# Optimization experiments

Measured on AMD Instinct MI355X. Metric: run time of the kernel, lower is better.

## Reference

```python
import jax, jax.numpy as jnp
import numpy as np

D_MODEL = 1024
NUM_HEADS = 16
D_K = D_MODEL // NUM_HEADS


def setup_inputs() -> dict:
    key = jax.random.key(0)
    ks = jax.random.split(key, 11)
    B, S, D = 2, 2048, D_MODEL
    scale = 1.0 / np.sqrt(D)
    inp = {
        'query': jax.random.normal(ks[0], (B, S, D), jnp.float32),
        'key':   jax.random.normal(ks[1], (B, S, D), jnp.float32),
        'value': jax.random.normal(ks[2], (B, S, D), jnp.float32),
        'Wq': jax.random.normal(ks[3], (D, D), jnp.float32) * scale,
        'bq': jnp.zeros((D,), jnp.float32),
        'Wk': jax.random.normal(ks[4], (D, D), jnp.float32) * scale,
        'bk': jnp.zeros((D,), jnp.float32),
        'Wv': jax.random.normal(ks[5], (D, D), jnp.float32) * scale,
        'bv': jnp.zeros((D,), jnp.float32),
        'Wo': jax.random.normal(ks[6], (D, D), jnp.float32) * scale,
        'bo': jnp.zeros((D,), jnp.float32),
    }
    return inp


def reference(query, key, value, Wq, bq, Wk, bk, Wv, bv, Wo, bo):
    B, S, D = query.shape
    H, dk = NUM_HEADS, D_K
    # QKV projections (torch Linear: x @ W.T + b)
    Q = (query @ Wq.T + bq).reshape(B, S, H, dk).transpose(0, 2, 1, 3)  # [B,H,S,dk]
    K = (key   @ Wk.T + bk).reshape(B, S, H, dk).transpose(0, 2, 1, 3)
    V = (value @ Wv.T + bv).reshape(B, S, H, dk).transpose(0, 2, 1, 3)
    # scaled dot-product attention; note: scaling uses d_k = per-head dim
    scores = jnp.einsum('bhqd,bhkd->bhqk', Q, K) / jnp.sqrt(jnp.float32(dk))
    attn = jax.nn.softmax(scores, axis=-1)  # [B,H,S,S]
    out = jnp.einsum('bhqk,bhkd->bhqd', attn, V)  # [B,H,S,dk]
    out = out.transpose(0, 2, 1, 3).reshape(B, S, D)
    return out @ Wo.T + bo
```

## Files before the change

kernel.cpp:

```cpp
#include <hip/hip_runtime.h>
#include <hip/hip_bf16.h>

#define S_LEN 2048
#define DM 1024
#define NH 16
#define DKH 64
#define BATCH 2

typedef __attribute__((ext_vector_type(4))) float f32x4;
typedef __attribute__((ext_vector_type(8))) short s16x8;
typedef __attribute__((ext_vector_type(4))) short s16x4;

__device__ __forceinline__ unsigned short f2bf(float f) {
    union { __hip_bfloat16 h; unsigned short u; } cv;
    cv.h = __float2bfloat16(f);
    return cv.u;
}

__device__ __forceinline__ void gl_lds16(const unsigned short* g, unsigned short* l) {
    __builtin_amdgcn_global_load_lds(
        (const __attribute__((address_space(1))) unsigned int*)g,
        (__attribute__((address_space(3))) unsigned int*)l,
        16, 0, 0);
}

__global__ __launch_bounds__(256) void cast_w(
    const float* __restrict__ w0, const float* __restrict__ w1,
    const float* __restrict__ w2, const float* __restrict__ w3,
    unsigned short* __restrict__ dst)
{
    const float* s = (blockIdx.y == 0) ? w0 : (blockIdx.y == 1) ? w1 : (blockIdx.y == 2) ? w2 : w3;
    unsigned short* d = dst + (size_t)blockIdx.y * (1024 * 1024);
    const int i = (blockIdx.x * 256 + threadIdx.x) * 8;
    float4 a = *(const float4*)(s + i), b = *(const float4*)(s + i + 4);
    s16x8 v;
    v[0] = f2bf(a.x); v[1] = f2bf(a.y); v[2] = f2bf(a.z); v[3] = f2bf(a.w);
    v[4] = f2bf(b.x); v[5] = f2bf(b.y); v[6] = f2bf(b.z); v[7] = f2bf(b.w);
    *(s16x8*)(d + i) = v;
}

__global__ __launch_bounds__(256) void qkv_gemm(
    const float* __restrict__ xq, const float* __restrict__ xk, const float* __restrict__ xv,
    const unsigned short* __restrict__ Wb,
    const float* __restrict__ bq, const float* __restrict__ bk, const float* __restrict__ bv,
    unsigned short* __restrict__ Qb, unsigned short* __restrict__ Kb,
    unsigned short* __restrict__ Vt)
{
    __shared__ __align__(16) unsigned short Al[128 * 32];
    __shared__ __align__(16) unsigned short Bl[128 * 32];

    const int tid = threadIdx.x, lane = tid & 63, w = tid >> 6;
    const int bn = blockIdx.x;
    const int seg = bn >> 3;
    const int nl0 = (bn & 7) * 128;
    const int m0 = blockIdx.y * 128;

    const float* A           = (seg == 0) ? xq : (seg == 1) ? xk : xv;
    const unsigned short* W  = Wb + (size_t)seg * 1024 * 1024;
    const float* bias        = (seg == 0) ? bq : (seg == 1) ? bk : bv;

    const int ar = tid >> 1, ac = (tid & 1) * 16;
    const int br = lane >> 2, bc = (lane & 3) * 8;
    const int wm = (w >> 1) * 64, wn = (w & 1) * 64;

    f32x4 acc[4][4] = {};

    for (int k0 = 0; k0 < DM; k0 += 32) {
        __syncthreads();
        #pragma unroll
        for (int j = 0; j < 2; j++) {
            const unsigned short* g = W + (size_t)(nl0 + w * 32 + j * 16 + br) * DM + k0 + bc;
            gl_lds16(g, &Bl[(w * 32 + j * 16) * 32]);
        }
        {
            const float* s = A + (size_t)(m0 + ar) * DM + k0 + ac;
            float4 x0 = *(const float4*)s,       x1 = *(const float4*)(s + 4);
            float4 x2 = *(const float4*)(s + 8), x3 = *(const float4*)(s + 12);
            s16x8 lo, hi;
            lo[0]=f2bf(x0.x); lo[1]=f2bf(x0.y); lo[2]=f2bf(x0.z); lo[3]=f2bf(x0.w);
            lo[4]=f2bf(x1.x); lo[5]=f2bf(x1.y); lo[6]=f2bf(x1.z); lo[7]=f2bf(x1.w);
            hi[0]=f2bf(x2.x); hi[1]=f2bf(x2.y); hi[2]=f2bf(x2.z); hi[3]=f2bf(x2.w);
            hi[4]=f2bf(x3.x); hi[5]=f2bf(x3.y); hi[6]=f2bf(x3.z); hi[7]=f2bf(x3.w);
            *(s16x8*)&Al[ar * 32 + ac] = lo;
            *(s16x8*)&Al[ar * 32 + ac + 8] = hi;
        }
        __syncthreads();

        const int kk = (lane >> 4) << 3;
        s16x8 af[4], bfr[4];
        #pragma unroll
        for (int i = 0; i < 4; i++) af[i]  = *(const s16x8*)&Al[(wm + i * 16 + (lane & 15)) * 32 + kk];
        #pragma unroll
        for (int i = 0; i < 4; i++) bfr[i] = *(const s16x8*)&Bl[(wn + i * 16 + (lane & 15)) * 32 + kk];
        #pragma unroll
        for (int i = 0; i < 4; i++)
            #pragma unroll
            for (int j = 0; j < 4; j++)
                acc[i][j] = __builtin_amdgcn_mfma_f32_16x16x32_bf16(af[i], bfr[j], acc[i][j], 0, 0, 0);
    }

    float bvv[4];
    #pragma unroll
    for (int ni = 0; ni < 4; ni++) bvv[ni] = bias[nl0 + wn + ni * 16 + (lane & 15)];

    if (seg < 2) {
        unsigned short* O = (seg == 0) ? Qb : Kb;
        #pragma unroll
        for (int mi = 0; mi < 4; mi++) {
            const int r0 = m0 + wm + mi * 16 + ((lane >> 4) << 2);
            #pragma unroll
            for (int ni = 0; ni < 4; ni++) {
                const int cg = nl0 + wn + ni * 16 + (lane & 15);
                #pragma unroll
                for (int r = 0; r < 4; r++)
                    O[(size_t)(r0 + r) * DM + cg] = f2bf(acc[mi][ni][r] + bvv[ni]);
            }
        }
    } else {
        #pragma unroll
        for (int mi = 0; mi < 4; mi++) {
            const int r0 = m0 + wm + mi * 16 + ((lane >> 4) << 2);
            const int bb = r0 >> 11, ss = r0 & (S_LEN - 1);
            #pragma unroll
            for (int ni = 0; ni < 4; ni++) {
                const int cg = nl0 + wn + ni * 16 + (lane & 15);
                const int hh = cg >> 6, dd = cg & 63;
                s16x4 vv;
                #pragma unroll
                for (int r = 0; r < 4; r++) vv[r] = (short)f2bf(acc[mi][ni][r] + bvv[ni]);
                *(s16x4*)(Vt + ((size_t)(bb * NH + hh) * DKH + dd) * S_LEN + ss) = vv;
            }
        }
    }
}

__global__ __launch_bounds__(512) void attn_k(
    const unsigned short* Qb, const unsigned short* __restrict__ Kb,
    const unsigned short* __restrict__ Vt, unsigned short* ctx)
{
    constexpr int KP = 72;
    __shared__ __align__(16) unsigned short Kl[2][64 * KP];
    __shared__ __align__(16) unsigned short Vl[2][64 * KP];
    __shared__ __align__(16) unsigned short Pl[8][16 * KP];

    const int tid = threadIdx.x, lane = tid & 63, w = tid >> 6;
    const int b = blockIdx.z, h = blockIdx.y, q0 = blockIdx.x * 128;
    const size_t qkb = (size_t)b * S_LEN * DM + h * DKH;
    const size_t vtb = (size_t)(b * NH + h) * DKH * S_LEN;

    s16x8 qf[2];
    {
        const int qr = q0 + w * 16 + (lane & 15);
        const unsigned short* qp = Qb + qkb + (size_t)qr * DM + ((lane >> 4) << 3);
        qf[0] = *(const s16x8*)qp;
        qf[1] = *(const s16x8*)(qp + 32);
    }

    f32x4 o[4] = {};
    float lp[4] = {0.f, 0.f, 0.f, 0.f};
    const int sr = tid >> 3, sc = (tid & 7) * 8;

    const float K1 = 0.18033688011112042f;
    const float K2 = 17.31234049066756f;

    s16x8 kreg = *(const s16x8*)(Kb + qkb + (size_t)sr * DM + sc);
    s16x8 vreg = *(const s16x8*)(Vt + vtb + (size_t)sr * S_LEN + sc);
    *(s16x8*)&Kl[0][sr * KP + sc] = kreg;
    *(s16x8*)&Vl[0][sr * KP + sc] = vreg;
    __syncthreads();
    int cur = 0;

    for (int t = 0; t < S_LEN / 64; ++t) {
        if (t < S_LEN / 64 - 1) {
            kreg = *(const s16x8*)(Kb + qkb + (size_t)((t + 1) * 64 + sr) * DM + sc);
            vreg = *(const s16x8*)(Vt + vtb + (size_t)sr * S_LEN + (t + 1) * 64 + sc);
        }
        const int kk = (lane >> 4) << 3;
        f32x4 sv[4] = {};
        #pragma unroll
        for (int c = 0; c < 2; c++) {
            #pragma unroll
            for (int f = 0; f < 4; f++) {
                s16x8 kf = *(const s16x8*)&Kl[cur][(f * 16 + (lane & 15)) * KP + c * 32 + kk];
                sv[f] = __builtin_amdgcn_mfma_f32_16x16x32_bf16(qf[c], kf, sv[f], 0, 0, 0);
            }
        }
        float p[4][4];
        #pragma unroll
        for (int f = 0; f < 4; f++)
            #pragma unroll
            for (int r = 0; r < 4; r++)
                p[f][r] = exp2f(fmaf(sv[f][r], K1, -K2));
        #pragma unroll
        for (int r = 0; r < 4; r++)
            lp[r] += (p[0][r] + p[1][r]) + (p[2][r] + p[3][r]);
        #pragma unroll
        for (int f = 0; f < 4; f++)
            #pragma unroll
            for (int r = 0; r < 4; r++)
                Pl[w][(((lane >> 4) << 2) + r) * KP + f * 16 + (lane & 15)] = f2bf(p[f][r]);
        #pragma unroll
        for (int c = 0; c < 2; c++) {
            s16x8 pa = *(const s16x8*)&Pl[w][(lane & 15) * KP + c * 32 + kk];
            #pragma unroll
            for (int j = 0; j < 4; j++) {
                s16x8 vf = *(const s16x8*)&Vl[cur][(j * 16 + (lane & 15)) * KP + c * 32 + kk];
                o[j] = __builtin_amdgcn_mfma_f32_16x16x32_bf16(pa, vf, o[j], 0, 0, 0);
            }
        }
        if (t < S_LEN / 64 - 1) {
            *(s16x8*)&Kl[cur ^ 1][sr * KP + sc] = kreg;
            *(s16x8*)&Vl[cur ^ 1][sr * KP + sc] = vreg;
        }
        __syncthreads();
        cur ^= 1;
    }

    float inv[4];
    #pragma unroll
    for (int r = 0; r < 4; r++) {
        float l = lp[r];
        l += __shfl_xor(l, 1); l += __shfl_xor(l, 2);
        l += __shfl_xor(l, 4); l += __shfl_xor(l, 8);
        inv[r] = 1.0f / l;
    }
    #pragma unroll
    for (int r = 0; r < 4; r++)
        #pragma unroll
        for (int j = 0; j < 4; j++)
            Pl[w][(((lane >> 4) << 2) + r) * KP + j * 16 + (lane & 15)] = f2bf(o[j][r] * inv[r]);
    {
        const int rr = lane >> 2, cc = (lane & 3) * 16;
        s16x8 a  = *(const s16x8*)&Pl[w][rr * KP + cc];
        s16x8 b2 = *(const s16x8*)&Pl[w][rr * KP + cc + 8];
        unsigned short* cp = ctx + (size_t)b * S_LEN * DM + (size_t)(q0 + w * 16 + rr) * DM + h * DKH + cc;
        *(s16x8*)cp = a; *(s16x8*)(cp + 8) = b2;
    }
}

__global__ __launch_bounds__(256) void out_gemm(
    const unsigned short* __restrict__ ctx, const unsigned short* __restrict__ Wo2,
    const float* __restrict__ bo, float* __restrict__ out)
{
    __shared__ __align__(16) unsigned short Al[128 * 32];
    __shared__ __align__(16) unsigned short Bl[128 * 32];

    const int tid = threadIdx.x, lane = tid & 63, w = tid >> 6;
    const int wm = (w >> 1) * 64, wn = (w & 1) * 64;
    const int m0 = blockIdx.y * 128, n0 = blockIdx.x * 128;
    const int br = lane >> 2, bc = (lane & 3) * 8;

    f32x4 acc[4][4] = {};

    for (int k0 = 0; k0 < DM; k0 += 32) {
        __syncthreads();
        #pragma unroll
        for (int j = 0; j < 2; j++) {
            gl_lds16(ctx + (size_t)(m0 + w * 32 + j * 16 + br) * DM + k0 + bc,
                     &Al[(w * 32 + j * 16) * 32]);
            gl_lds16(Wo2 + (size_t)(n0 + w * 32 + j * 16 + br) * DM + k0 + bc,
                     &Bl[(w * 32 + j * 16) * 32]);
        }
        __syncthreads();

        const int kk = (lane >> 4) << 3;
        s16x8 af[4], bfr[4];
        #pragma unroll
        for (int i = 0; i < 4; i++) af[i]  = *(const s16x8*)&Al[(wm + i * 16 + (lane & 15)) * 32 + kk];
        #pragma unroll
        for (int i = 0; i < 4; i++) bfr[i] = *(const s16x8*)&Bl[(wn + i * 16 + (lane & 15)) * 32 + kk];
        #pragma unroll
        for (int i = 0; i < 4; i++)
            #pragma unroll
            for (int j = 0; j < 4; j++)
                acc[i][j] = __builtin_amdgcn_mfma_f32_16x16x32_bf16(af[i], bfr[j], acc[i][j], 0, 0, 0);
    }

    float bvv[4];
    #pragma unroll
    for (int ni = 0; ni < 4; ni++) bvv[ni] = bo[n0 + wn + ni * 16 + (lane & 15)];
    #pragma unroll
    for (int mi = 0; mi < 4; mi++) {
        const int r0 = m0 + wm + mi * 16 + ((lane >> 4) << 2);
        #pragma unroll
        for (int ni = 0; ni < 4; ni++) {
            const int cg = n0 + wn + ni * 16 + (lane & 15);
            #pragma unroll
            for (int r = 0; r < 4; r++)
                out[(size_t)(r0 + r) * DM + cg] = acc[mi][ni][r] + bvv[ni];
        }
    }
}

extern "C" void kernel_launch(void* const* d_in, const int* in_sizes, int n_in,
                              void* d_out, int out_size, void* d_ws, size_t ws_size,
                              hipStream_t stream) {
    const float* q  = (const float*)d_in[0];
    const float* k  = (const float*)d_in[1];
    const float* v  = (const float*)d_in[2];
    const float* Wq = (const float*)d_in[3];
    const float* bq = (const float*)d_in[4];
    const float* Wk = (const float*)d_in[5];
    const float* bk = (const float*)d_in[6];
    const float* Wv = (const float*)d_in[7];
    const float* bv = (const float*)d_in[8];
    const float* Wo = (const float*)d_in[9];
    const float* bo = (const float*)d_in[10];

    const size_t NE = (size_t)BATCH * S_LEN * DM;
    unsigned short* Kb = (unsigned short*)d_ws;
    unsigned short* Vt = Kb + NE;
    unsigned short* Qb = Vt + NE;
    unsigned short* Wb = Qb + NE;
    float* out = (float*)d_out;

    cast_w<<<dim3(512, 4), 256, 0, stream>>>(Wq, Wk, Wv, Wo, Wb);
    qkv_gemm<<<dim3(24, 32), 256, 0, stream>>>(q, k, v, Wb, bq, bk, bv, Qb, Kb, Vt);
    attn_k<<<dim3(16, NH, BATCH), 512, 0, stream>>>(Qb, Kb, Vt, Qb );
    out_gemm<<<dim3(8, 32), 256, 0, stream>>>(Qb , Wb + 3 * 1024 * 1024, bo, out);
}
```

Before: 263.4 us.

## Swizzle LDS layouts, async-load attention tiles, precast inputs, shrink output GEMM tile

Replaces the padded and unswizzled LDS layouts with XOR-swizzled layouts in every GEMM and in attention, which targets LDS bank conflicts. Attention now streams K/V tiles with direct global-to-LDS loads instead of going through registers, and raises wave priority around the MFMA sections. When the workspace is large enough, a separate kernel casts the inputs to bf16 so the QKV GEMM can use global_load_lds for both operands. The output GEMM tile is cut to 128x64 to launch more blocks. The extra cast pass adds a kernel launch and extra memory traffic, and the precast path only runs if the workspace size check passes.

Measured after the change: 243.7 us. 1.08x faster.

```diff
diff --git a/kernel.cpp b/kernel.cpp
--- a/kernel.cpp
+++ b/kernel.cpp
@@ -22,6 +22,22 @@
         (const __attribute__((address_space(1))) unsigned int*)g,
         (__attribute__((address_space(3))) unsigned int*)l,
         16, 0, 0);
+}
+
+__device__ __forceinline__ int a32(int row, int col) {
+    return row * 32 + ((((col >> 3) ^ ((row >> 1) & 3)) & 3) << 3) + (col & 7);
+}
+__device__ __forceinline__ int csw32(int l) {
+    return (((l & 3) ^ ((l >> 3) & 3)) << 3);
+}
+__device__ __forceinline__ int a64(int row, int col) {
+    return row * 64 + ((((col >> 3) ^ (row & 7)) & 7) << 3) + (col & 7);
+}
+__device__ __forceinline__ int csw64(int l) {
+    return (((l & 7) ^ ((l >> 3) & 7)) << 3);
+}
+__device__ __forceinline__ int pswz(int row, int col) {
+    return row * 72 + (col ^ ((row & 8) << 1));
 }
 
 __global__ __launch_bounds__(256) void cast_w(
@@ -39,7 +55,108 @@
     *(s16x8*)(d + i) = v;
 }
 
-__global__ __launch_bounds__(256) void qkv_gemm(
+__global__ __launch_bounds__(256) void cast_x(
+    const float* __restrict__ x0, const float* __restrict__ x1, const float* __restrict__ x2,
+    unsigned short* __restrict__ dst)
+{
+    const float* s = (blockIdx.y == 0) ? x0 : (blockIdx.y == 1) ? x1 : x2;
+    unsigned short* d = dst + (size_t)blockIdx.y * ((size_t)BATCH * S_LEN * DM);
+    const int i = (blockIdx.x * 256 + threadIdx.x) * 8;
+    float4 a = *(const float4*)(s + i), b = *(const float4*)(s + i + 4);
+    s16x8 v;
+    v[0] = f2bf(a.x); v[1] = f2bf(a.y); v[2] = f2bf(a.z); v[3] = f2bf(a.w);
+    v[4] = f2bf(b.x); v[5] = f2bf(b.y); v[6] = f2bf(b.z); v[7] = f2bf(b.w);
+    *(s16x8*)(d + i) = v;
+}
+
+__device__ __forceinline__ void qkv_store(
+    int seg, int m0, int nl0, int wm, int wn, int lane,
+    f32x4 acc[4][4],
+    const float* bq, const float* bk, const float* bv,
+    unsigned short* Qb, unsigned short* Kb, unsigned short* Vt)
+{
+    const float* bias = (seg == 0) ? bq : (seg == 1) ? bk : bv;
+    float bvv[4];
+    #pragma unroll
+    for (int ni = 0; ni < 4; ni++) bvv[ni] = bias[nl0 + wn + ni * 16 + (lane & 15)];
+
+    if (seg < 2) {
+        unsigned short* O = (seg == 0) ? Qb : Kb;
+        #pragma unroll
+        for (int mi = 0; mi < 4; mi++) {
+            const int r0 = m0 + wm + mi * 16 + ((lane >> 4) << 2);
+            #pragma unroll
+            for (int ni = 0; ni < 4; ni++) {
+                const int cg = nl0 + wn + ni * 16 + (lane & 15);
+                #pragma unroll
+                for (int r = 0; r < 4; r++)
+                    O[(size_t)(r0 + r) * DM + cg] = f2bf(acc[mi][ni][r] + bvv[ni]);
+            }
+        }
+    } else {
+        #pragma unroll
+        for (int mi = 0; mi < 4; mi++) {
+            const int r0 = m0 + wm + mi * 16 + ((lane >> 4) << 2);
+            const int bb = r0 >> 11, ss = r0 & (S_LEN - 1);
+            #pragma unroll
+            for (int ni = 0; ni < 4; ni++) {
+                const int cg = nl0 + wn + ni * 16 + (lane & 15);
+                const int hh = cg >> 6, dd = cg & 63;
+                s16x4 vv;
+                #pragma unroll
+                for (int r = 0; r < 4; r++) vv[r] = (short)f2bf(acc[mi][ni][r] + bvv[ni]);
+                *(s16x4*)(Vt + ((size_t)(bb * NH + hh) * DKH + dd) * S_LEN + ss) = vv;
+            }
+        }
+    }
+}
+
+__global__ __launch_bounds__(256) void qkv_pre(
+    const unsigned short* __restrict__ Xb, const unsigned short* __restrict__ Wb,
+    const float* __restrict__ bq, const float* __restrict__ bk, const float* __restrict__ bv,
+    unsigned short* __restrict__ Qb, unsigned short* __restrict__ Kb,
+    unsigned short* __restrict__ Vt)
+{
+    __shared__ __align__(16) unsigned short Al[128 * 32];
+    __shared__ __align__(16) unsigned short Bl[128 * 32];
+
+    const int tid = threadIdx.x, lane = tid & 63, w = tid >> 6;
+    const int seg = blockIdx.x >> 3, nl0 = (blockIdx.x & 7) * 128, m0 = blockIdx.y * 128;
+    const unsigned short* A = Xb + (size_t)seg * ((size_t)BATCH * S_LEN * DM);
+    const unsigned short* W = Wb + (size_t)seg * 1024 * 1024;
+
+    const int srow = lane >> 2, scol = csw32(lane);
+    const int wm = (w >> 1) * 64, wn = (w & 1) * 64;
+    const int l4 = lane & 15, kk = (lane >> 4) << 3;
+
+    f32x4 acc[4][4] = {};
+
+    for (int k0 = 0; k0 < DM; k0 += 32) {
+        __syncthreads();
+        #pragma unroll
+        for (int j = 0; j < 2; j++) {
+            gl_lds16(A + (size_t)(m0 + w * 32 + j * 16 + srow) * DM + k0 + scol,
+                     &Al[(w * 32 + j * 16) * 32]);
+            gl_lds16(W + (size_t)(nl0 + w * 32 + j * 16 + srow) * DM + k0 + scol,
+                     &Bl[(w * 32 + j * 16) * 32]);
+        }
+        __syncthreads();
+
+        s16x8 af[4], bfr[4];
+        #pragma unroll
+        for (int i = 0; i < 4; i++) af[i]  = *(const s16x8*)&Al[a32(wm + i * 16 + l4, kk)];
+        #pragma unroll
+        for (int i = 0; i < 4; i++) bfr[i] = *(const s16x8*)&Bl[a32(wn + i * 16 + l4, kk)];
+        #pragma unroll
+        for (int i = 0; i < 4; i++)
+            #pragma unroll
+            for (int j = 0; j < 4; j++)
+                acc[i][j] = __builtin_amdgcn_mfma_f32_16x16x32_bf16(af[i], bfr[j], acc[i][j], 0, 0, 0);
+    }
+    qkv_store(seg, m0, nl0, wm, wn, lane, acc, bq, bk, bv, Qb, Kb, Vt);
+}
+
+__global__ __launch_bounds__(256) void qkv_f32(
     const float* __restrict__ xq, const float* __restrict__ xk, const float* __restrict__ xv,
     const unsigned short* __restrict__ Wb,
     const float* __restrict__ bq, const float* __restrict__ bk, const float* __restrict__ bv,
@@ -50,28 +167,23 @@
     __shared__ __align__(16) unsigned short Bl[128 * 32];
 
     const int tid = threadIdx.x, lane = tid & 63, w = tid >> 6;
-    const int bn = blockIdx.x;
-    const int seg = bn >> 3;
-    const int nl0 = (bn & 7) * 128;
-    const int m0 = blockIdx.y * 128;
-
-    const float* A           = (seg == 0) ? xq : (seg == 1) ? xk : xv;
-    const unsigned short* W  = Wb + (size_t)seg * 1024 * 1024;
-    const float* bias        = (seg == 0) ? bq : (seg == 1) ? bk : bv;
-
+    const int seg = blockIdx.x >> 3, nl0 = (blockIdx.x & 7) * 128, m0 = blockIdx.y * 128;
+    const float* A          = (seg == 0) ? xq : (seg == 1) ? xk : xv;
+    const unsigned short* W = Wb + (size_t)seg * 1024 * 1024;
+
+    const int srow = lane >> 2, scol = csw32(lane);
     const int ar = tid >> 1, ac = (tid & 1) * 16;
-    const int br = lane >> 2, bc = (lane & 3) * 8;
     const int wm = (w >> 1) * 64, wn = (w & 1) * 64;
+    const int l4 = lane & 15, kk = (lane >> 4) << 3;
 
     f32x4 acc[4][4] = {};
 
     for (int k0 = 0; k0 < DM; k0 += 32) {
         __syncthreads();
         #pragma unroll
-        for (int j = 0; j < 2; j++) {
-            const unsigned short* g = W + (size_t)(nl0 + w * 32 + j * 16 + br) * DM + k0 + bc;
-            gl_lds16(g, &Bl[(w * 32 + j * 16) * 32]);
-        }
+        for (int j = 0; j < 2; j++)
+            gl_lds16(W + (size_t)(nl0 + w * 32 + j * 16 + srow) * DM + k0 + scol,
+                     &Bl[(w * 32 + j * 16) * 32]);
         {
             const float* s = A + (size_t)(m0 + ar) * DM + k0 + ac;
             float4 x0 = *(const float4*)s,       x1 = *(const float4*)(s + 4);
@@ -81,110 +193,76 @@
             lo[4]=f2bf(x1.x); lo[5]=f2bf(x1.y); lo[6]=f2bf(x1.z); lo[7]=f2bf(x1.w);
             hi[0]=f2bf(x2.x); hi[1]=f2bf(x2.y); hi[2]=f2bf(x2.z); hi[3]=f2bf(x2.w);
             hi[4]=f2bf(x3.x); hi[5]=f2bf(x3.y); hi[6]=f2bf(x3.z); hi[7]=f2bf(x3.w);
-            *(s16x8*)&Al[ar * 32 + ac] = lo;
-            *(s16x8*)&Al[ar * 32 + ac + 8] = hi;
-        }
-        __syncthreads();
-
-        const int kk = (lane >> 4) << 3;
+            *(s16x8*)&Al[a32(ar, ac)] = lo;
+            *(s16x8*)&Al[a32(ar, ac + 8)] = hi;
+        }
+        __syncthreads();
+
         s16x8 af[4], bfr[4];
         #pragma unroll
-        for (int i = 0; i < 4; i++) af[i]  = *(const s16x8*)&Al[(wm + i * 16 + (lane & 15)) * 32 + kk];
-        #pragma unroll
-        for (int i = 0; i < 4; i++) bfr[i] = *(const s16x8*)&Bl[(wn + i * 16 + (lane & 15)) * 32 + kk];
+        for (int i = 0; i < 4; i++) af[i]  = *(const s16x8*)&Al[a32(wm + i * 16 + l4, kk)];
+        #pragma unroll
+        for (int i = 0; i < 4; i++) bfr[i] = *(const s16x8*)&Bl[a32(wn + i * 16 + l4, kk)];
         #pragma unroll
         for (int i = 0; i < 4; i++)
             #pragma unroll
             for (int j = 0; j < 4; j++)
                 acc[i][j] = __builtin_amdgcn_mfma_f32_16x16x32_bf16(af[i], bfr[j], acc[i][j], 0, 0, 0);
     }
-
-    float bvv[4];
-    #pragma unroll
-    for (int ni = 0; ni < 4; ni++) bvv[ni] = bias[nl0 + wn + ni * 16 + (lane & 15)];
-
-    if (seg < 2) {
-        unsigned short* O = (seg == 0) ? Qb : Kb;
-        #pragma unroll
-        for (int mi = 0; mi < 4; mi++) {
-            const int r0 = m0 + wm + mi * 16 + ((lane >> 4) << 2);
-            #pragma unroll
-            for (int ni = 0; ni < 4; ni++) {
-                const int cg = nl0 + wn + ni * 16 + (lane & 15);
-                #pragma unroll
-                for (int r = 0; r < 4; r++)
-                    O[(size_t)(r0 + r) * DM + cg] = f2bf(acc[mi][ni][r] + bvv[ni]);
-            }
-        }
-    } else {
-        #pragma unroll
-        for (int mi = 0; mi < 4; mi++) {
-            const int r0 = m0 + wm + mi * 16 + ((lane >> 4) << 2);
-            const int bb = r0 >> 11, ss = r0 & (S_LEN - 1);
-            #pragma unroll
-            for (int ni = 0; ni < 4; ni++) {
-                const int cg = nl0 + wn + ni * 16 + (lane & 15);
-                const int hh = cg >> 6, dd = cg & 63;
-                s16x4 vv;
-                #pragma unroll
-                for (int r = 0; r < 4; r++) vv[r] = (short)f2bf(acc[mi][ni][r] + bvv[ni]);
-                *(s16x4*)(Vt + ((size_t)(bb * NH + hh) * DKH + dd) * S_LEN + ss) = vv;
-            }
-        }
-    }
+    qkv_store(seg, m0, nl0, wm, wn, lane, acc, bq, bk, bv, Qb, Kb, Vt);
 }
 
 __global__ __launch_bounds__(512) void attn_k(
     const unsigned short* Qb, const unsigned short* __restrict__ Kb,
     const unsigned short* __restrict__ Vt, unsigned short* ctx)
 {
-    constexpr int KP = 72;
-    __shared__ __align__(16) unsigned short Kl[2][64 * KP];
-    __shared__ __align__(16) unsigned short Vl[2][64 * KP];
-    __shared__ __align__(16) unsigned short Pl[8][16 * KP];
+    __shared__ __align__(16) unsigned short Kl[2][64 * 64];
+    __shared__ __align__(16) unsigned short Vl[2][64 * 64];
+    __shared__ __align__(16) unsigned short Pl[8][16 * 72];
 
     const int tid = threadIdx.x, lane = tid & 63, w = tid >> 6;
     const int b = blockIdx.z, h = blockIdx.y, q0 = blockIdx.x * 128;
     const size_t qkb = (size_t)b * S_LEN * DM + h * DKH;
     const size_t vtb = (size_t)(b * NH + h) * DKH * S_LEN;
+    const int l4 = lane & 15, kk = (lane >> 4) << 3;
 
     s16x8 qf[2];
     {
-        const int qr = q0 + w * 16 + (lane & 15);
-        const unsigned short* qp = Qb + qkb + (size_t)qr * DM + ((lane >> 4) << 3);
+        const int qr = q0 + w * 16 + l4;
+        const unsigned short* qp = Qb + qkb + (size_t)qr * DM + kk;
         qf[0] = *(const s16x8*)qp;
         qf[1] = *(const s16x8*)(qp + 32);
     }
 
     f32x4 o[4] = {};
     float lp[4] = {0.f, 0.f, 0.f, 0.f};
-    const int sr = tid >> 3, sc = (tid & 7) * 8;
+    const int srow = w * 8 + (lane >> 3);
+    const int scol = csw64(lane);
 
     const float K1 = 0.18033688011112042f;
     const float K2 = 17.31234049066756f;
 
-    s16x8 kreg = *(const s16x8*)(Kb + qkb + (size_t)sr * DM + sc);
-    s16x8 vreg = *(const s16x8*)(Vt + vtb + (size_t)sr * S_LEN + sc);
-    *(s16x8*)&Kl[0][sr * KP + sc] = kreg;
-    *(s16x8*)&Vl[0][sr * KP + sc] = vreg;
+    gl_lds16(Kb + qkb + (size_t)srow * DM + scol,  &Kl[0][w * 512]);
+    gl_lds16(Vt + vtb + (size_t)srow * S_LEN + scol, &Vl[0][w * 512]);
     __syncthreads();
     int cur = 0;
 
     for (int t = 0; t < S_LEN / 64; ++t) {
         if (t < S_LEN / 64 - 1) {
-            kreg = *(const s16x8*)(Kb + qkb + (size_t)((t + 1) * 64 + sr) * DM + sc);
-            vreg = *(const s16x8*)(Vt + vtb + (size_t)sr * S_LEN + (t + 1) * 64 + sc);
-        }
-        const int kk = (lane >> 4) << 3;
+            gl_lds16(Kb + qkb + (size_t)((t + 1) * 64 + srow) * DM + scol, &Kl[cur ^ 1][w * 512]);
+            gl_lds16(Vt + vtb + (size_t)srow * S_LEN + (t + 1) * 64 + scol, &Vl[cur ^ 1][w * 512]);
+        }
         f32x4 sv[4] = {};
+        __builtin_amdgcn_s_setprio(1);
         #pragma unroll
         for (int c = 0; c < 2; c++) {
             #pragma unroll
             for (int f = 0; f < 4; f++) {
-                s16x8 kf = *(const s16x8*)&Kl[cur][(f * 16 + (lane & 15)) * KP + c * 32 + kk];
+                s16x8 kf = *(const s16x8*)&Kl[cur][a64(f * 16 + l4, c * 32 + kk)];
                 sv[f] = __builtin_amdgcn_mfma_f32_16x16x32_bf16(qf[c], kf, sv[f], 0, 0, 0);
             }
         }
+        __builtin_amdgcn_s_setprio(0);
         float p[4][4];
         #pragma unroll
         for (int f = 0; f < 4; f++)
@@ -198,20 +276,18 @@
         for (int f = 0; f < 4; f++)
             #pragma unroll
             for (int r = 0; r < 4; r++)
-                Pl[w][(((lane >> 4) << 2) + r) * KP + f * 16 + (lane & 15)] = f2bf(p[f][r]);
+                Pl[w][pswz(((lane >> 4) << 2) + r, f * 16 + l4)] = f2bf(p[f][r]);
+        __builtin_amdgcn_s_setprio(1);
         #pragma unroll
         for (int c = 0; c < 2; c++) {
-            s16x8 pa = *(const s16x8*)&Pl[w][(lane & 15) * KP + c * 32 + kk];
+            s16x8 pa = *(const s16x8*)&Pl[w][pswz(l4, c * 32 + kk)];
             #pragma unroll
             for (int j = 0; j < 4; j++) {
-                s16x8 vf = *(const s16x8*)&Vl[cur][(j * 16 + (lane & 15)) * KP + c * 32 + kk];
+                s16x8 vf = *(const s16x8*)&Vl[cur][a64(j * 16 + l4, c * 32 + kk)];
                 o[j] = __builtin_amdgcn_mfma_f32_16x16x32_bf16(pa, vf, o[j], 0, 0, 0);
             }
         }
-        if (t < S_LEN / 64 - 1) {
-            *(s16x8*)&Kl[cur ^ 1][sr * KP + sc] = kreg;
-            *(s16x8*)&Vl[cur ^ 1][sr * KP + sc] = vreg;
-        }
+        __builtin_amdgcn_s_setprio(0);
         __syncthreads();
         cur ^= 1;
     }
@@ -228,11 +304,11 @@
     for (int r = 0; r < 4; r++)
         #pragma unroll
         for (int j = 0; j < 4; j++)
-            Pl[w][(((lane >> 4) << 2) + r) * KP + j * 16 + (lane & 15)] = f2bf(o[j][r] * inv[r]);
+            Pl[w][pswz(((lane >> 4) << 2) + r, j * 16 + l4)] = f2bf(o[j][r] * inv[r]);
     {
         const int rr = lane >> 2, cc = (lane & 3) * 16;
-        s16x8 a  = *(const s16x8*)&Pl[w][rr * KP + cc];
-        s16x8 b2 = *(const s16x8*)&Pl[w][rr * KP + cc + 8];
+        s16x8 a  = *(const s16x8*)&Pl[w][pswz(rr, cc)];
+        s16x8 b2 = *(const s16x8*)&Pl[w][pswz(rr, cc + 8)];
         unsigned short* cp = ctx + (size_t)b * S_LEN * DM + (size_t)(q0 + w * 16 + rr) * DM + h * DKH + cc;
         *(s16x8*)cp = a; *(s16x8*)(cp + 8) = b2;
     }
@@ -243,48 +319,47 @@
     const float* __restrict__ bo, float* __restrict__ out)
 {
     __shared__ __align__(16) unsigned short Al[128 * 32];
-    __shared__ __align__(16) unsigned short Bl[128 * 32];
+    __shared__ __align__(16) unsigned short Bl[64 * 32];
 
     const int tid = threadIdx.x, lane = tid & 63, w = tid >> 6;
-    const int wm = (w >> 1) * 64, wn = (w & 1) * 64;
-    const int m0 = blockIdx.y * 128, n0 = blockIdx.x * 128;
-    const int br = lane >> 2, bc = (lane & 3) * 8;
-
-    f32x4 acc[4][4] = {};
+    const int wm = (w >> 1) * 64, wn = (w & 1) * 32;
+    const int n0 = blockIdx.x * 64, m0 = blockIdx.y * 128;
+    const int srow = lane >> 2, scol = csw32(lane);
+    const int l4 = lane & 15, kk = (lane >> 4) << 3;
+
+    f32x4 acc[4][2] = {};
 
     for (int k0 = 0; k0 < DM; k0 += 32) {
         __syncthreads();
         #pragma unroll
-        for (int j = 0; j < 2; j++) {
-            gl_lds16(ctx + (size_t)(m0 + w * 32 + j * 16 + br) * DM + k0 + bc,
+        for (int j = 0; j < 2; j++)
+            gl_lds16(ctx + (size_t)(m0 + w * 32 + j * 16 + srow) * DM + k0 + scol,
                      &Al[(w * 32 + j * 16) * 32]);
-            gl_lds16(Wo2 + (size_t)(n0 + w * 32 + j * 16 + br) * DM + k0 + bc,
-                     &Bl[(w * 32 + j * 16) * 32]);
-        }
-        __syncthreads();
-
-        const int kk = (lane >> 4) << 3;
-        s16x8 af[4], bfr[4];
-        #pragma unroll
-        for (int i = 0; i < 4; i++) af[i]  = *(const s16x8*)&Al[(wm + i * 16 + (lane & 15)) * 32 + kk];
-        #pragma unroll
-        for (int i = 0; i < 4; i++) bfr[i] = *(const s16x8*)&Bl[(wn + i * 16 + (lane & 15)) * 32 + kk];
+        gl_lds16(Wo2 + (size_t)(n0 + w * 16 + srow) * DM + k0 + scol,
+                 &Bl[(w * 16) * 32]);
+        __syncthreads();
+
+        s16x8 af[4], bfr[2];
+        #pragma unroll
+        for (int i = 0; i < 4; i++) af[i]  = *(const s16x8*)&Al[a32(wm + i * 16 + l4, kk)];
+        #pragma unroll
+        for (int i = 0; i < 2; i++) bfr[i] = *(const s16x8*)&Bl[a32(wn + i * 16 + l4, kk)];
         #pragma unroll
         for (int i = 0; i < 4; i++)
             #pragma unroll
-            for (int j = 0; j < 4; j++)
+            for (int j = 0; j < 2; j++)
                 acc[i][j] = __builtin_amdgcn_mfma_f32_16x16x32_bf16(af[i], bfr[j], acc[i][j], 0, 0, 0);
     }
 
-    float bvv[4];
+    float bvv[2];
     #pragma unroll
-    for (int ni = 0; ni < 4; ni++) bvv[ni] = bo[n0 + wn + ni * 16 + (lane & 15)];
+    for (int ni = 0; ni < 2; ni++) bvv[ni] = bo[n0 + wn + ni * 16 + l4];
     #pragma unroll
     for (int mi = 0; mi < 4; mi++) {
         const int r0 = m0 + wm + mi * 16 + ((lane >> 4) << 2);
         #pragma unroll
-        for (int ni = 0; ni < 4; ni++) {
-            const int cg = n0 + wn + ni * 16 + (lane & 15);
+        for (int ni = 0; ni < 2; ni++) {
+            const int cg = n0 + wn + ni * 16 + l4;
             #pragma unroll
             for (int r = 0; r < 4; r++)
                 out[(size_t)(r0 + r) * DM + cg] = acc[mi][ni][r] + bvv[ni];
@@ -312,10 +387,18 @@
     unsigned short* Vt = Kb + NE;
     unsigned short* Qb = Vt + NE;
     unsigned short* Wb = Qb + NE;
+    unsigned short* Xb = Wb + 4 * 1024 * 1024;
     float* out = (float*)d_out;
 
+    const bool precast = ws_size >= (size_t)56 * 1024 * 1024;
+
     cast_w<<<dim3(512, 4), 256, 0, stream>>>(Wq, Wk, Wv, Wo, Wb);
-    qkv_gemm<<<dim3(24, 32), 256, 0, stream>>>(q, k, v, Wb, bq, bk, bv, Qb, Kb, Vt);
+    if (precast) {
+        cast_x<<<dim3(2048, 3), 256, 0, stream>>>(q, k, v, Xb);
+        qkv_pre<<<dim3(24, 32), 256, 0, stream>>>(Xb, Wb, bq, bk, bv, Qb, Kb, Vt);
+    } else {
+        qkv_f32<<<dim3(24, 32), 256, 0, stream>>>(q, k, v, Wb, bq, bk, bv, Qb, Kb, Vt);
+    }
     attn_k<<<dim3(16, NH, BATCH), 512, 0, stream>>>(Qb, Kb, Vt, Qb );
-    out_gemm<<<dim3(8, 32), 256, 0, stream>>>(Qb , Wb + 3 * 1024 * 1024, bo, out);
-}
+    out_gemm<<<dim3(16, 32), 256, 0, stream>>>(Qb , Wb + 3 * 1024 * 1024, bo, out);
+}
```
